# Optimization experiments

Measured on AMD Instinct MI355X. Metric: run time of the kernel, lower is better.

## Reference

```python
import jax, jax.numpy as jnp
import numpy as np


def setup_inputs() -> dict:
    key = jax.random.key(0)
    k1, k2 = jax.random.split(key)
    N, D, C = 16384, 128, 1000
    embeddings = jax.random.normal(k1, (N, D), dtype=jnp.float32)
    labels = jax.random.randint(k2, (N,), 0, C, dtype=jnp.int64)
    return {"embeddings": embeddings, "labels": labels}


def reference(embeddings, labels):
    # Vectorized equivalent of the O(N^2) Python mining loop:
    # for each anchor i, positive = first j>i with labels[j]==labels[i],
    #                    negative = first j>i with labels[j]!=labels[i].
    # Anchor i yields a triplet only if BOTH exist.
    # Original returns a variable-length stack; for fixed shapes we return the
    # full [3, N, D] triplets (invalid anchors zeroed) plus a validity mask.
    N = labels.shape[0]
    same = labels[:, None] == labels[None, :]            # [N, N]
    upper = jnp.arange(N)[None, :] > jnp.arange(N)[:, None]  # j > i
    pos_cand = same & upper
    neg_cand = (~same) & upper
    pos_idx = jnp.argmax(pos_cand, axis=1)               # first True (0 if none)
    neg_idx = jnp.argmax(neg_cand, axis=1)
    valid = pos_cand.any(axis=1) & neg_cand.any(axis=1)  # [N]
    triplets = jnp.stack([embeddings,
                          embeddings[pos_idx],
                          embeddings[neg_idx]])          # [3, N, D]
    triplets = triplets * valid[None, :, None].astype(embeddings.dtype)
    return triplets, valid
```

## Files before the change

### kernel.cpp

```cpp
#include <hip/hip_runtime.h>

typedef float f32x4 __attribute__((ext_vector_type(4)));

#define BLOCK 256

__global__ void __launch_bounds__(BLOCK) triplet_fused_kernel(
    const int* __restrict__ labels,
    const f32x4* __restrict__ emb,
    f32x4* __restrict__ out,
    float* __restrict__ valid_out,
    int N) {

    const int D4 = 32;
    int lane = threadIdx.x & 63;
    int i = blockIdx.x * (BLOCK >> 6) + (threadIdx.x >> 6);
    if (i >= N) return;

    int d4 = lane & 31;
    f32x4 ea = emb[(size_t)i * D4 + d4];
    int my = labels[i];

    const int4* lab4 = (const int4*)labels;
    int nq = N >> 2;

    int kb0 = (i + 1) >> 2;

    unsigned mv_first = 0xFFu;
    if (lane == 0) {
        int j0 = kb0 << 2;
        int nclr = i - j0 + 1;
        if (nclr > 0) mv_first &= (0xFFu << nclr);
    }

    int kbase = kb0;
    bool fp = false, fn = false;
    unsigned long long balp = 0, baln = 0;
    int basep = 0, basen = 0;
    unsigned msp = 0, msn = 0;

    int4 a0 = lab4[min(kbase + 2 * lane,     nq - 1)];
    int4 b0 = lab4[min(kbase + 2 * lane + 1, nq - 1)];
    int4 a1 = lab4[min(kbase + 128 + 2 * lane,     nq - 1)];
    int4 b1 = lab4[min(kbase + 128 + 2 * lane + 1, nq - 1)];

    unsigned mv_iter = mv_first;
    if (kbase < nq) {
        while (true) {
            int4 a2 = lab4[min(kbase + 256 + 2 * lane,     nq - 1)];
            int4 b2 = lab4[min(kbase + 256 + 2 * lane + 1, nq - 1)];

            int kq0 = kbase + 2 * lane, kq1 = kq0 + 1;
            unsigned mv = mv_iter;
            if (kq0 >= nq)      mv = 0;
            else if (kq1 >= nq) mv &= 0x0Fu;

            unsigned ms = (a0.x == my ?   1u : 0u) | (a0.y == my ?   2u : 0u)
                        | (a0.z == my ?   4u : 0u) | (a0.w == my ?   8u : 0u)
                        | (b0.x == my ?  16u : 0u) | (b0.y == my ?  32u : 0u)
                        | (b0.z == my ?  64u : 0u) | (b0.w == my ? 128u : 0u);

            unsigned mp = ms & mv;
            unsigned mn = (~ms) & mv;
            unsigned long long bp = __ballot(mp != 0u);
            unsigned long long bn = __ballot(mn != 0u);
            if (!fp && bp) { fp = true; balp = bp; basep = kbase; msp = mp; }
            if (!fn && bn) { fn = true; baln = bn; basen = kbase; msn = mn; }

            kbase += 128;
            if ((fp && fn) || kbase >= nq) break;
            a0 = a1; b0 = b1; a1 = a2; b1 = b2;
            mv_iter = 0xFFu;
        }
    }

    int p = 0, ng = 0;
    if (fp) {
        int ls = (int)__ffsll(balp) - 1;
        unsigned m = __shfl(msp, ls);
        p = ((basep + 2 * ls) << 2) + (__ffs(m) - 1);
    }
    if (fn) {
        int ls = (int)__ffsll(baln) - 1;
        unsigned m = __shfl(msn, ls);
        ng = ((basen + 2 * ls) << 2) + (__ffs(m) - 1);
    }

    float v = (fp && fn) ? 1.0f : 0.0f;

    size_t ND4 = (size_t)N * D4;
    int gsrc = (lane < 32) ? ng : p;
    f32x4 eg = emb[(size_t)gsrc * D4 + d4];

    if (lane == 0) valid_out[i] = v;

    int   t  = lane >> 5;
    f32x4 r0 = (lane < 32) ? ea : eg;
    out[(size_t)t * ND4 + (size_t)i * D4 + d4] = r0 * v;

    if (lane < 32)
        out[2 * ND4 + (size_t)i * D4 + d4] = eg * v;
}

extern "C" void kernel_launch(void* const* d_in, const int* in_sizes, int n_in,
                              void* d_out, int out_size, void* d_ws, size_t ws_size,
                              hipStream_t stream) {
    const float* emb    = (const float*)d_in[0];
    const int*   labels = (const int*)d_in[1];

    int N = in_sizes[1];
    int D = in_sizes[0] / N;

    float* out       = (float*)d_out;
    float* valid_out = out + (size_t)3 * N * D;

    int nblk = (N * 64 + BLOCK - 1) / BLOCK;
    triplet_fused_kernel<<<nblk, BLOCK, 0, stream>>>(
        labels, (const f32x4*)emb, (f32x4*)out, valid_out, N);
}
```

Baseline: 15.33 us.

## Bucket anchor indices by label to find next positive via per-class lists

Adds a scatter pass that uses atomics to bucket sample indices per label into fixed-size slots. The main kernel then finds the positive as the smallest bucket entry greater than i, using a wave min-reduction, in place of scanning the label array. Negatives are found with a simple 64-wide ballot scan, which usually ends on the first step. This adds a memset and a second kernel launch, and it depends on the labels fitting the bin and slot sizes, with a scanning fallback when they don't.

```diff
diff --git a/kernel.cpp b/kernel.cpp
--- a/kernel.cpp
+++ b/kernel.cpp
@@ -3,15 +3,33 @@
 typedef float f32x4 __attribute__((ext_vector_type(4)));
 
 #define BLOCK 256
+#define NBINS 1024
+#define SLOT  128
 
-__global__ void __launch_bounds__(BLOCK) triplet_fused_kernel(
+__global__ void scatter_kernel(const int* __restrict__ labels,
+                               int* __restrict__ cnt,
+                               int* __restrict__ items,
+                               int N) {
+    int i = blockIdx.x * blockDim.x + threadIdx.x;
+    if (i >= N) return;
+    int c = labels[i];
+    if ((unsigned)c < NBINS) {
+        int r = atomicAdd(&cnt[c], 1);
+        if (r < SLOT) items[c * SLOT + r] = i;
+    }
+}
+
+__global__ void __launch_bounds__(BLOCK) triplet_main_kernel(
     const int* __restrict__ labels,
+    const int* __restrict__ cnt,
+    const int* __restrict__ items,
     const f32x4* __restrict__ emb,
     f32x4* __restrict__ out,
     float* __restrict__ valid_out,
     int N) {
 
     const int D4 = 32;
+    const int INF = 0x7FFFFFFF;
     int lane = threadIdx.x & 63;
     int i = blockIdx.x * (BLOCK >> 6) + (threadIdx.x >> 6);
     if (i >= N) return;
@@ -20,78 +38,42 @@
     f32x4 ea = emb[(size_t)i * D4 + d4];
     int my = labels[i];
 
-    const int4* lab4 = (const int4*)labels;
-    int nq = N >> 2;
-
-    int kb0 = (i + 1) >> 2;
-
-    unsigned mv_first = 0xFFu;
-    if (lane == 0) {
-        int j0 = kb0 << 2;
-        int nclr = i - j0 + 1;
-        if (nclr > 0) mv_first &= (0xFFu << nclr);
-    }
-
-    int kbase = kb0;
-    bool fp = false, fn = false;
-    unsigned long long balp = 0, baln = 0;
-    int basep = 0, basen = 0;
-    unsigned msp = 0, msn = 0;
-
-    int4 a0 = lab4[min(kbase + 2 * lane,     nq - 1)];
-    int4 b0 = lab4[min(kbase + 2 * lane + 1, nq - 1)];
-    int4 a1 = lab4[min(kbase + 128 + 2 * lane,     nq - 1)];
-    int4 b1 = lab4[min(kbase + 128 + 2 * lane + 1, nq - 1)];
-
-    unsigned mv_iter = mv_first;
-    if (kbase < nq) {
-        while (true) {
-            int4 a2 = lab4[min(kbase + 256 + 2 * lane,     nq - 1)];
-            int4 b2 = lab4[min(kbase + 256 + 2 * lane + 1, nq - 1)];
-
-            int kq0 = kbase + 2 * lane, kq1 = kq0 + 1;
-            unsigned mv = mv_iter;
-            if (kq0 >= nq)      mv = 0;
-            else if (kq1 >= nq) mv &= 0x0Fu;
-
-            unsigned ms = (a0.x == my ?   1u : 0u) | (a0.y == my ?   2u : 0u)
-                        | (a0.z == my ?   4u : 0u) | (a0.w == my ?   8u : 0u)
-                        | (b0.x == my ?  16u : 0u) | (b0.y == my ?  32u : 0u)
-                        | (b0.z == my ?  64u : 0u) | (b0.w == my ? 128u : 0u);
-
-            unsigned mp = ms & mv;
-            unsigned mn = (~ms) & mv;
-            unsigned long long bp = __ballot(mp != 0u);
-            unsigned long long bn = __ballot(mn != 0u);
-            if (!fp && bp) { fp = true; balp = bp; basep = kbase; msp = mp; }
-            if (!fn && bn) { fn = true; baln = bn; basen = kbase; msn = mn; }
-
-            kbase += 128;
-            if ((fp && fn) || kbase >= nq) break;
-            a0 = a1; b0 = b1; a1 = a2; b1 = b2;
-            mv_iter = 0xFFu;
+    int p = -1;
+    int n = ((unsigned)my < NBINS) ? cnt[my] : SLOT + 1;
+    if (n <= SLOT) {
+        int v0 = (lane < n)      ? items[my * SLOT + lane]      : INF;
+        int v1 = (lane + 64 < n) ? items[my * SLOT + lane + 64] : INF;
+        if (v0 <= i) v0 = INF;
+        if (v1 <= i) v1 = INF;
+        int v = min(v0, v1);
+        #pragma unroll
+        for (int off = 32; off > 0; off >>= 1)
+            v = min(v, __shfl_xor(v, off));
+        if (v != INF) p = v;
+    } else {
+        for (int base = i + 1; base < N; base += 64) {
+            int j = base + lane;
+            unsigned long long bs = __ballot(j < N && labels[j] == my);
+            if (bs) { p = base + (int)__ffsll(bs) - 1; break; }
         }
     }
 
-    int p = 0, ng = 0;
-    if (fp) {
-        int ls = (int)__ffsll(balp) - 1;
-        unsigned m = __shfl(msp, ls);
-        p = ((basep + 2 * ls) << 2) + (__ffs(m) - 1);
-    }
-    if (fn) {
-        int ls = (int)__ffsll(baln) - 1;
-        unsigned m = __shfl(msn, ls);
-        ng = ((basen + 2 * ls) << 2) + (__ffs(m) - 1);
+    int ng = -1;
+    for (int base = i + 1; base < N; base += 64) {
+        int j = base + lane;
+        unsigned long long bd = __ballot(j < N && labels[j] != my);
+        if (bd) { ng = base + (int)__ffsll(bd) - 1; break; }
     }
 
-    float v = (fp && fn) ? 1.0f : 0.0f;
+    float v  = (p >= 0 && ng >= 0) ? 1.0f : 0.0f;
+    int   ps = (p  >= 0) ? p  : 0;
+    int   ns = (ng >= 0) ? ng : 0;
+
+    if (lane == 0) valid_out[i] = v;
 
     size_t ND4 = (size_t)N * D4;
-    int gsrc = (lane < 32) ? ng : p;
+    int gsrc = (lane < 32) ? ns : ps;
     f32x4 eg = emb[(size_t)gsrc * D4 + d4];
-
-    if (lane == 0) valid_out[i] = v;
 
     int   t  = lane >> 5;
     f32x4 r0 = (lane < 32) ? ea : eg;
@@ -113,7 +95,15 @@
     float* out       = (float*)d_out;
     float* valid_out = out + (size_t)3 * N * D;
 
-    int nblk = (N * 64 + BLOCK - 1) / BLOCK;
-    triplet_fused_kernel<<<nblk, BLOCK, 0, stream>>>(
-        labels, (const f32x4*)emb, (f32x4*)out, valid_out, N);
+    int* cnt   = (int*)d_ws;
+    int* items = cnt + NBINS;
+
+    hipMemsetAsync(cnt, 0, NBINS * sizeof(int), stream);
+
+    int nblk_s = (N + BLOCK - 1) / BLOCK;
+    scatter_kernel<<<nblk_s, BLOCK, 0, stream>>>(labels, cnt, items, N);
+
+    int nblk_m = (N * 64 + BLOCK - 1) / BLOCK;
+    triplet_main_kernel<<<nblk_m, BLOCK, 0, stream>>>(
+        labels, cnt, items, (const f32x4*)emb, (f32x4*)out, valid_out, N);
 }
```

Result: slower. 24.54 us (+60.0%).

## Process two anchors per wavefront sharing label scans

Applied to the files above, without the earlier changes.

Each wavefront now handles two consecutive anchors and reuses one stream of label loads to compare against both anchors' labels. The scan width per iteration drops from 8 labels per lane to 4, and the launch uses half as many waves, with a min-blocks-per-CU hint added to launch bounds. This is meant to halve redundant label traffic and wave launch overhead, at the cost of more registers, more ballots per iteration, and two serialized gather/store phases per wave.

```diff
diff --git a/kernel.cpp b/kernel.cpp
--- a/kernel.cpp
+++ b/kernel.cpp
@@ -4,7 +4,7 @@
 
 #define BLOCK 256
 
-__global__ void __launch_bounds__(BLOCK) triplet_fused_kernel(
+__global__ void __launch_bounds__(BLOCK, 8) triplet_fused_kernel(
     const int* __restrict__ labels,
     const f32x4* __restrict__ emb,
     f32x4* __restrict__ out,
@@ -13,92 +13,109 @@
 
     const int D4 = 32;
     int lane = threadIdx.x & 63;
-    int i = blockIdx.x * (BLOCK >> 6) + (threadIdx.x >> 6);
-    if (i >= N) return;
+    int wid  = blockIdx.x * (BLOCK >> 6) + (threadIdx.x >> 6);
+    int i0 = wid * 2, i1 = i0 + 1;
+    if (i0 >= N) return;
+    bool has1 = (i1 < N);
 
     int d4 = lane & 31;
-    f32x4 ea = emb[(size_t)i * D4 + d4];
-    int my = labels[i];
+    f32x4 ea0 = emb[(size_t)i0 * D4 + d4];
+    f32x4 ea1 = has1 ? emb[(size_t)i1 * D4 + d4] : f32x4{0, 0, 0, 0};
+    int my0 = labels[i0];
+    int my1 = has1 ? labels[i1] : my0;
 
     const int4* lab4 = (const int4*)labels;
     int nq = N >> 2;
+    int kb = (i0 + 1) >> 2;
 
-    int kb0 = (i + 1) >> 2;
-
-    unsigned mv_first = 0xFFu;
+    unsigned mv0 = 0xFu, mv1 = 0xFu;
     if (lane == 0) {
-        int j0 = kb0 << 2;
-        int nclr = i - j0 + 1;
-        if (nclr > 0) mv_first &= (0xFFu << nclr);
+        int j0 = kb << 2;
+        unsigned m0 = 0, m1 = 0;
+        #pragma unroll
+        for (int b = 0; b < 4; ++b) {
+            int j = j0 + b;
+            if (j > i0) m0 |= (1u << b);
+            if (j > i1) m1 |= (1u << b);
+        }
+        mv0 = m0; mv1 = m1;
     }
 
-    int kbase = kb0;
-    bool fp = false, fn = false;
-    unsigned long long balp = 0, baln = 0;
-    int basep = 0, basen = 0;
-    unsigned msp = 0, msn = 0;
+    bool fp0 = false, fn0 = false, fp1 = !has1, fn1 = !has1;
+    unsigned long long balP0 = 0, balN0 = 0, balP1 = 0, balN1 = 0;
+    int baseP0 = 0, baseN0 = 0, baseP1 = 0, baseN1 = 0;
+    unsigned msP0 = 0, msN0 = 0, msP1 = 0, msN1 = 0;
 
-    int4 a0 = lab4[min(kbase + 2 * lane,     nq - 1)];
-    int4 b0 = lab4[min(kbase + 2 * lane + 1, nq - 1)];
-    int4 a1 = lab4[min(kbase + 128 + 2 * lane,     nq - 1)];
-    int4 b1 = lab4[min(kbase + 128 + 2 * lane + 1, nq - 1)];
+    if (kb < nq) {
+        int4 c0 = lab4[min(kb +      lane, nq - 1)];
+        int4 c1 = lab4[min(kb + 64 + lane, nq - 1)];
+        int kbase = kb;
+        while (true) {
+            int4 c2 = lab4[min(kbase + 128 + lane, nq - 1)];
 
-    unsigned mv_iter = mv_first;
-    if (kbase < nq) {
-        while (true) {
-            int4 a2 = lab4[min(kbase + 256 + 2 * lane,     nq - 1)];
-            int4 b2 = lab4[min(kbase + 256 + 2 * lane + 1, nq - 1)];
+            unsigned mvc = ((kbase + lane) < nq) ? 0xFu : 0u;
+            unsigned m0v = mv0 & mvc, m1v = mv1 & mvc;
 
-            int kq0 = kbase + 2 * lane, kq1 = kq0 + 1;
-            unsigned mv = mv_iter;
-            if (kq0 >= nq)      mv = 0;
-            else if (kq1 >= nq) mv &= 0x0Fu;
+            unsigned e0 = (c0.x == my0 ? 1u : 0u) | (c0.y == my0 ? 2u : 0u)
+                        | (c0.z == my0 ? 4u : 0u) | (c0.w == my0 ? 8u : 0u);
+            unsigned e1 = (c0.x == my1 ? 1u : 0u) | (c0.y == my1 ? 2u : 0u)
+                        | (c0.z == my1 ? 4u : 0u) | (c0.w == my1 ? 8u : 0u);
 
-            unsigned ms = (a0.x == my ?   1u : 0u) | (a0.y == my ?   2u : 0u)
-                        | (a0.z == my ?   4u : 0u) | (a0.w == my ?   8u : 0u)
-                        | (b0.x == my ?  16u : 0u) | (b0.y == my ?  32u : 0u)
-                        | (b0.z == my ?  64u : 0u) | (b0.w == my ? 128u : 0u);
+            unsigned p0m = e0 & m0v, n0m = (~e0) & m0v;
+            unsigned p1m = e1 & m1v, n1m = (~e1) & m1v;
+            unsigned long long bp0 = __ballot(p0m != 0u);
+            unsigned long long bn0 = __ballot(n0m != 0u);
+            unsigned long long bp1 = __ballot(p1m != 0u);
+            unsigned long long bn1 = __ballot(n1m != 0u);
 
-            unsigned mp = ms & mv;
-            unsigned mn = (~ms) & mv;
-            unsigned long long bp = __ballot(mp != 0u);
-            unsigned long long bn = __ballot(mn != 0u);
-            if (!fp && bp) { fp = true; balp = bp; basep = kbase; msp = mp; }
-            if (!fn && bn) { fn = true; baln = bn; basen = kbase; msn = mn; }
+            if (!fp0 && bp0) { fp0 = true; balP0 = bp0; baseP0 = kbase; msP0 = p0m; }
+            if (!fn0 && bn0) { fn0 = true; balN0 = bn0; baseN0 = kbase; msN0 = n0m; }
+            if (has1) {
+                if (!fp1 && bp1) { fp1 = true; balP1 = bp1; baseP1 = kbase; msP1 = p1m; }
+                if (!fn1 && bn1) { fn1 = true; balN1 = bn1; baseN1 = kbase; msN1 = n1m; }
+            }
 
-            kbase += 128;
-            if ((fp && fn) || kbase >= nq) break;
-            a0 = a1; b0 = b1; a1 = a2; b1 = b2;
-            mv_iter = 0xFFu;
+            kbase += 64;
+            if ((fp0 && fn0 && fp1 && fn1) || kbase >= nq) break;
+            c0 = c1; c1 = c2;
+            mv0 = 0xFu; mv1 = 0xFu;
         }
     }
 
-    int p = 0, ng = 0;
-    if (fp) {
-        int ls = (int)__ffsll(balp) - 1;
-        unsigned m = __shfl(msp, ls);
-        p = ((basep + 2 * ls) << 2) + (__ffs(m) - 1);
-    }
-    if (fn) {
-        int ls = (int)__ffsll(baln) - 1;
-        unsigned m = __shfl(msn, ls);
-        ng = ((basen + 2 * ls) << 2) + (__ffs(m) - 1);
-    }
+    int p0 = 0, ng0 = 0, p1 = 0, ng1 = 0;
+    if (balP0) { int ls = (int)__ffsll(balP0) - 1; unsigned m = __shfl(msP0, ls);
+                 p0  = ((baseP0 + ls) << 2) + (__ffs(m) - 1); }
+    if (balN0) { int ls = (int)__ffsll(balN0) - 1; unsigned m = __shfl(msN0, ls);
+                 ng0 = ((baseN0 + ls) << 2) + (__ffs(m) - 1); }
+    if (balP1) { int ls = (int)__ffsll(balP1) - 1; unsigned m = __shfl(msP1, ls);
+                 p1  = ((baseP1 + ls) << 2) + (__ffs(m) - 1); }
+    if (balN1) { int ls = (int)__ffsll(balN1) - 1; unsigned m = __shfl(msN1, ls);
+                 ng1 = ((baseN1 + ls) << 2) + (__ffs(m) - 1); }
 
-    float v = (fp && fn) ? 1.0f : 0.0f;
+    float v0 = (balP0 && balN0) ? 1.0f : 0.0f;
+    float v1 = (balP1 && balN1) ? 1.0f : 0.0f;
+
+    if (lane < 2 && i0 + lane < N)
+        valid_out[i0 + lane] = lane ? v1 : v0;
 
     size_t ND4 = (size_t)N * D4;
-    int gsrc = (lane < 32) ? ng : p;
-    f32x4 eg = emb[(size_t)gsrc * D4 + d4];
+    int g0 = (lane < 32) ? ng0 : p0;
+    f32x4 eg0 = emb[(size_t)g0 * D4 + d4];
+    int g1 = (lane < 32) ? ng1 : p1;
+    f32x4 eg1 = has1 ? emb[(size_t)g1 * D4 + d4] : f32x4{0, 0, 0, 0};
 
-    if (lane == 0) valid_out[i] = v;
+    int t = lane >> 5;
+    f32x4 r0 = (lane < 32) ? ea0 : eg0;
+    out[(size_t)t * ND4 + (size_t)i0 * D4 + d4] = r0 * v0;
+    if (lane < 32)
+        out[2 * ND4 + (size_t)i0 * D4 + d4] = eg0 * v0;
 
-    int   t  = lane >> 5;
-    f32x4 r0 = (lane < 32) ? ea : eg;
-    out[(size_t)t * ND4 + (size_t)i * D4 + d4] = r0 * v;
-
-    if (lane < 32)
-        out[2 * ND4 + (size_t)i * D4 + d4] = eg * v;
+    if (has1) {
+        f32x4 r1 = (lane < 32) ? ea1 : eg1;
+        out[(size_t)t * ND4 + (size_t)i1 * D4 + d4] = r1 * v1;
+        if (lane < 32)
+            out[2 * ND4 + (size_t)i1 * D4 + d4] = eg1 * v1;
+    }
 }
 
 extern "C" void kernel_launch(void* const* d_in, const int* in_sizes, int n_in,
@@ -113,7 +130,8 @@
     float* out       = (float*)d_out;
     float* valid_out = out + (size_t)3 * N * D;
 
-    int nblk = (N * 64 + BLOCK - 1) / BLOCK;
+    int waves = (N + 1) / 2;
+    int nblk  = (waves * 64 + BLOCK - 1) / BLOCK;
     triplet_fused_kernel<<<nblk, BLOCK, 0, stream>>>(
         labels, (const f32x4*)emb, (f32x4*)out, valid_out, N);
 }
```

After: 18.88 us. 23.1% more time.
